# Optimization experiments

Measured on AMD Instinct MI355X. Metric: run time of the kernel, lower is better.

Reference implementation:

```python
import jax, jax.numpy as jnp
import numpy as np

N, E, MUL, ATTR, NBASIS = 30000, 480000, 32, 8, 8
AVG_NEIGH = 16.0
INV_SQRT3 = 1.0 / np.sqrt(3.0).astype(np.float32)  # wigner 3j (1,1,0)
LOG2 = float(np.log(2.0))


def ssp(x):
    # shifted softplus: softplus(x) - log(2)
    return jax.nn.softplus(x) - LOG2


def setup_inputs() -> dict:
    key = jax.random.key(0)
    ks = jax.random.split(key, 15)
    return {
        "node_s": jax.random.normal(ks[0], (N, MUL), jnp.float32),
        "node_v": jax.random.normal(ks[1], (N, MUL, 3), jnp.float32),
        "node_attr": jax.random.uniform(ks[2], (N, ATTR), jnp.float32),
        "edge_attr": jax.random.normal(ks[3], (E, 4), jnp.float32),       # [sh0 | sh1(3)]
        "edge_scalars": jax.random.uniform(ks[4], (E, NBASIS), jnp.float32),
        "W1_0": jax.random.normal(ks[5], (MUL, MUL), jnp.float32),
        "W1_1": jax.random.normal(ks[6], (MUL, MUL), jnp.float32),
        "Wfc1": jax.random.normal(ks[7], (NBASIS, NBASIS), jnp.float32),
        "Wfc2": jax.random.normal(ks[8], (NBASIS, 4 * MUL), jnp.float32),
        "W2_0": jax.random.normal(ks[9], (2 * MUL, MUL), jnp.float32),
        "W2_1": jax.random.normal(ks[10], (2 * MUL, MUL), jnp.float32),
        "Wsc0": jax.random.normal(ks[11], (MUL, ATTR, MUL), jnp.float32),
        "Wsc1": jax.random.normal(ks[12], (MUL, ATTR, MUL), jnp.float32),
        "edge_src": jax.random.randint(ks[13], (E,), 0, N, jnp.int32),
        "edge_dst": jax.random.randint(ks[14], (E,), 0, N, jnp.int32),
    }


def reference(node_s, node_v, node_attr, edge_attr, edge_scalars,
              W1_0, W1_1, Wfc1, Wfc2, W2_0, W2_1, Wsc0, Wsc1,
              edge_src, edge_dst):
    n_nodes, mul = node_s.shape
    # --- fc: radial MLP -> per-edge TP weights (shared_weights=False) ---
    h = ssp(edge_scalars @ Wfc1 * (1.0 / np.sqrt(Wfc1.shape[0])))
    w = h @ Wfc2 * (1.0 / np.sqrt(Wfc2.shape[0]))                 # [E, 4*MUL]
    w00, w01, w10, w11 = jnp.split(w, 4, axis=1)                  # instruction order
    # --- lin1: per-irrep linear (fan-in normalized) ---
    inv_m = 1.0 / np.sqrt(mul)
    x0 = node_s @ W1_0 * inv_m                                    # [N, MUL]
    x1 = jnp.einsum('nud,uw->nwd', node_v, W1_1) * inv_m          # [N, MUL, 3]
    # --- gather destination-node features per edge ---
    x0d, x1d = x0[edge_dst], x1[edge_dst]
    sh0, sh1 = edge_attr[:, :1], edge_attr[:, 1:4]
    # --- uvu tensor product with per-edge weights ---
    s_a = w00 * x0d * sh0                                         # 0e x 0e -> 0e
    s_b = w11 * jnp.einsum('eud,ed->eu', x1d, sh1) * INV_SQRT3    # 1o x 1o -> 0e
    v_a = (w01 * x0d)[:, :, None] * sh1[:, None, :]               # 0e x 1o -> 1o
    v_b = w10[:, :, None] * x1d * sh0[:, :, None]                 # 1o x 0e -> 1o
    mid_s = jnp.concatenate([s_a, s_b], axis=1)                   # [E, 64]  (64x0e)
    mid_v = jnp.concatenate([v_a, v_b], axis=1)                   # [E, 64, 3] (64x1o)
    # --- scatter-sum over edge_src, normalized by sqrt(avg_num_neighbors) ---
    inv_nb = 1.0 / np.sqrt(AVG_NEIGH)
    agg_s = jax.ops.segment_sum(mid_s, edge_src, num_segments=n_nodes) * inv_nb
    agg_v = jax.ops.segment_sum(mid_v, edge_src, num_segments=n_nodes) * inv_nb
    # --- lin2 ---
    inv_2m = 1.0 / np.sqrt(2.0 * mul)
    out0 = agg_s @ W2_0 * inv_2m                                  # [N, MUL]
    out1 = jnp.einsum('nud,uw->nwd', agg_v, W2_1) * inv_2m        # [N, MUL, 3]
    # --- self-connection: fully-connected TP (attr is scalar 8x0e) ---
    sc_norm = 1.0 / np.sqrt(mul * node_attr.shape[1])
    sc0 = jnp.einsum('nu,nv,uvw->nw', node_s, node_attr, Wsc0) * sc_norm
    sc1 = jnp.einsum('nud,nv,uvw->nwd', node_v, node_attr, Wsc1) * sc_norm
    o0 = out0 + sc0
    o1 = out1 + sc1
    return jnp.concatenate([o0, o1.reshape(n_nodes, mul * 3)], axis=1)  # [N, 128]
```

## Files before the change

kernel.cpp:

```cpp
#include <hip/hip_runtime.h>
#include <math.h>

#define N_NODES 30000
#define N_EDGES 480000

typedef __attribute__((ext_vector_type(8))) short short8;
typedef __attribute__((ext_vector_type(4))) float f32x4;
typedef __attribute__((ext_vector_type(2))) float f32x2;

__device__ __forceinline__ unsigned short f2bf(float f) {
    unsigned u = __float_as_uint(f);
    u += 0x7fff + ((u >> 16) & 1);
    return (unsigned short)(u >> 16);
}
__device__ __forceinline__ float bfLO(unsigned v) { return __uint_as_float(v << 16); }
__device__ __forceinline__ float bfHI(unsigned v) { return __uint_as_float(v & 0xffff0000u); }
__device__ __forceinline__ unsigned packbf(float a, float b) {
    return (unsigned)f2bf(a) | ((unsigned)f2bf(b) << 16);
}
__device__ __forceinline__ unsigned ptk(float a, float b) {
    return (__float_as_uint(a) >> 16) | (__float_as_uint(b) & 0xffff0000u);
}

union U8 { short8 v; unsigned u[4]; };
union C4 { f32x4 v; float f[4]; };

__global__ __launch_bounds__(256) void k_count(
    const int* __restrict__ edge_src,
    int* __restrict__ deg,
    int* __restrict__ epos)
{
    int e = blockIdx.x * 256 + threadIdx.x;
    epos[e] = atomicAdd(&deg[edge_src[e]], 1);
}

__global__ __launch_bounds__(256) void k_pre(
    const float* __restrict__ node_s,
    const float* __restrict__ node_v,
    const float* __restrict__ W1_0,
    const float* __restrict__ W1_1,
    const float* __restrict__ Wsc0,
    const float* __restrict__ Wsc1,
    const float* __restrict__ W2_0,
    const float* __restrict__ W2_1,
    const int* __restrict__ deg,
    int* __restrict__ offs,
    unsigned short* __restrict__ xnode,
    unsigned* __restrict__ bsc0,
    unsigned* __restrict__ bsc1,
    unsigned* __restrict__ b20,
    unsigned* __restrict__ b21)
{
    __shared__ __align__(16) char smem[15360];
    __shared__ int wsb[6];
    float* sVT = (float*)smem;
    float* sXo = (float*)(smem + 6400);
    int*   sdg = (int*)smem;
    int tid = threadIdx.x;

    if (blockIdx.x == 0) {
        int lane = tid & 63, wid = tid >> 6;
        int running = 0;
        for (int c = 0; c < N_NODES; c += 3840) {
            int size = min(3840, N_NODES - c);
#pragma unroll
            for (int k = 0; k < 15; ++k) {
                int i = tid + k * 256;
                sdg[i] = (i < size) ? deg[c + i] : 0;
            }
            __syncthreads();
            int bt = tid * 15;
            int s = 0;
#pragma unroll
            for (int k = 0; k < 15; ++k) s += sdg[bt + k];
            int inc = s;
#pragma unroll
            for (int d = 1; d < 64; d <<= 1) {
                int o = __shfl_up(inc, d, 64);
                if (lane >= d) inc += o;
            }
            if (lane == 63) wsb[wid] = inc;
            __syncthreads();
            if (tid == 0) {
                int t0 = 0;
#pragma unroll
                for (int w = 0; w < 4; ++w) { int v = wsb[w]; wsb[w] = t0; t0 += v; }
                wsb[4] = t0;
            }
            __syncthreads();
            int run2 = inc - s + wsb[wid] + running;
#pragma unroll
            for (int k = 0; k < 15; ++k) {
                int idx = bt + k;
                int gi = c + idx;
                int d = sdg[idx];
                if (gi < N_NODES) offs[gi] = run2;
                run2 += d;
            }
            running += wsb[4];
            __syncthreads();
        }
        if (tid == 0) offs[N_NODES] = N_EDGES;
        return;
    }

    if (blockIdx.x >= 1876) {
        int b = blockIdx.x - 1876;
        const float* Wm = (b == 0) ? Wsc0 : (b == 1) ? Wsc1 : (b == 2) ? W2_0 : W2_1;
        unsigned* dst = (b == 0) ? bsc0 : (b == 1) ? bsc1 : (b == 2) ? b20 : b21;
        float scale = (b < 2) ? 0.0625f : 0.03125f;
        int nu = (b < 2) ? 4096 : 1024;
        for (int idx = tid; idx < nu; idx += 256) {
            int jp = idx & 3;
            int lane = (idx >> 2) & 63;
            int ft = (idx >> 8) & 1;
            int kc = idx >> 9;
            int quad = lane >> 4, col = lane & 15;
            int k = kc * 32 + quad * 8 + jp * 2;
            int c = ft * 16 + col;
            dst[idx] = packbf(Wm[k * 32 + c] * scale, Wm[(k + 1) * 32 + c] * scale);
        }
        return;
    }

    int nbase = (blockIdx.x - 1) * 16;
    for (int i = tid; i < 1536; i += 256) {
        int nl = i / 96, r = i - nl * 96;
        int u = r / 3, d = r - u * 3;
        sVT[nl * 100 + d * 32 + u] = node_v[(size_t)nbase * 96 + i];
    }
    __syncthreads();

    int lane = tid & 63;
    int wv = tid >> 6;
    int col = lane & 15, quad = lane >> 4, m = lane & 15;

    const float* W1 = (wv == 0) ? W1_0 : W1_1;
    U8 bf0, bf1;
#pragma unroll
    for (int p = 0; p < 4; ++p) {
        int k = quad * 8 + 2 * p;
        bf0.u[p] = packbf(W1[k * 32 + col],      W1[(k + 1) * 32 + col]);
        bf1.u[p] = packbf(W1[k * 32 + col + 16], W1[(k + 1) * 32 + col + 16]);
    }

    U8 af;
    if (wv == 0) {
        const float* sp = node_s + (size_t)(nbase + m) * 32 + quad * 8;
        float4 a0 = *(const float4*)(sp);
        float4 a1 = *(const float4*)(sp + 4);
        af.u[0] = packbf(a0.x, a0.y); af.u[1] = packbf(a0.z, a0.w);
        af.u[2] = packbf(a1.x, a1.y); af.u[3] = packbf(a1.z, a1.w);
    } else {
        int R = 16 * (wv - 1) + m;
        int nl = R / 3, d = R - nl * 3;
        const float* vp = sVT + nl * 100 + d * 32 + quad * 8;
        af.u[0] = packbf(vp[0], vp[1]); af.u[1] = packbf(vp[2], vp[3]);
        af.u[2] = packbf(vp[4], vp[5]); af.u[3] = packbf(vp[6], vp[7]);
    }

    f32x4 acc0 = {0.f, 0.f, 0.f, 0.f};
    f32x4 acc1 = {0.f, 0.f, 0.f, 0.f};
    acc0 = __builtin_amdgcn_mfma_f32_16x16x32_bf16(af.v, bf0.v, acc0, 0, 0, 0);
    acc1 = __builtin_amdgcn_mfma_f32_16x16x32_bf16(af.v, bf1.v, acc1, 0, 0, 0);

    C4 c0, c1;
    c0.v = acc0; c1.v = acc1;
    if (wv == 0) {
#pragma unroll
        for (int r = 0; r < 4; ++r) {
            int nl = (quad << 2) + r;
            sXo[nl * 140 + col]      = c0.f[r];
            sXo[nl * 140 + col + 16] = c1.f[r];
        }
    } else {
#pragma unroll
        for (int r = 0; r < 4; ++r) {
            int R = 16 * (wv - 1) + (quad << 2) + r;
            int nl = R / 3, d = R - nl * 3;
            sXo[nl * 140 + (1 + d) * 34 + col]      = c0.f[r];
            sXo[nl * 140 + (1 + d) * 34 + col + 16] = c1.f[r];
        }
    }
    __syncthreads();

    const float inv_m = 0.1767766953f;
    for (int i = tid; i < 512; i += 256) {
        int nl = i >> 5, u = i & 31;
        const float* xp = sXo + nl * 140;
        uint2 pk;
        pk.x = packbf(xp[u] * inv_m,       xp[34 + u] * inv_m);
        pk.y = packbf(xp[68 + u] * inv_m,  xp[102 + u] * inv_m);
        *(uint2*)(xnode + (size_t)(nbase + nl) * 128 + u * 4) = pk;
    }
}

__global__ __launch_bounds__(256) void fill_kernel(
    const float* __restrict__ edge_attr,
    const float* __restrict__ edge_scalars,
    const float* __restrict__ Wfc1,
    const int* __restrict__ edge_src,
    const int* __restrict__ edge_dst,
    const int* __restrict__ offs,
    const int* __restrict__ epos,
    uint4* __restrict__ rec)
{
    __shared__ float sW[64];
    int tid = threadIdx.x;
    if (tid < 64) sW[tid] = Wfc1[tid];
    __syncthreads();

    int e = blockIdx.x * 256 + tid;
    float4 es0 = *(const float4*)(edge_scalars + (size_t)e * 8);
    float4 es1 = *(const float4*)(edge_scalars + (size_t)e * 8 + 4);
    float4 ea  = *(const float4*)(edge_attr + (size_t)e * 4);
    int src = edge_src[e];
    int dst = edge_dst[e];
    int pos = offs[src] + epos[e];

    const float inv8 = 0.3535533906f;
    float h[8];
#pragma unroll
    for (int i = 0; i < 8; ++i) {
        float acc = es0.x * sW[0 * 8 + i];
        acc = fmaf(es0.y, sW[1 * 8 + i], acc);
        acc = fmaf(es0.z, sW[2 * 8 + i], acc);
        acc = fmaf(es0.w, sW[3 * 8 + i], acc);
        acc = fmaf(es1.x, sW[4 * 8 + i], acc);
        acc = fmaf(es1.y, sW[5 * 8 + i], acc);
        acc = fmaf(es1.z, sW[6 * 8 + i], acc);
        acc = fmaf(es1.w, sW[7 * 8 + i], acc);
        acc *= inv8;
        float ax = fabsf(acc);
        float tt = __expf(-ax);
        h[i] = fmaxf(acc, 0.f) + __logf(1.f + tt) - 0.6931471806f;
    }
    uint4 r0, r1;
    r0.x = packbf(h[0], h[1]); r0.y = packbf(h[2], h[3]);
    r0.z = packbf(h[4], h[5]); r0.w = packbf(h[6], h[7]);
    r1.x = packbf(ea.x, ea.y); r1.y = packbf(ea.z, ea.w);
    r1.z = ((unsigned)dst) << 8;
    r1.w = 0;
    rec[2 * pos]     = r0;
    rec[2 * pos + 1] = r1;
}

struct GAcc {
    float sa, sb, va2, vb2;
    f32x2 va01, vb01;
};

__device__ __forceinline__ void gstep(
    uint4& RS0, uint4& RS1, uint2& XS, const uint4& RN1, uint2& XN,
    int& t, int cntH, int& pf, int L,
    const char* recc, const char* xbc,
    const f32x2* wfA, const f32x2* wfB, GAcc& g)
{
    float hv[8];
    hv[0] = bfLO(RS0.x); hv[1] = bfHI(RS0.x);
    hv[2] = bfLO(RS0.y); hv[3] = bfHI(RS0.y);
    hv[4] = bfLO(RS0.z); hv[5] = bfHI(RS0.z);
    hv[6] = bfLO(RS0.w); hv[7] = bfHI(RS0.w);
    float sh0  = bfLO(RS1.x), s1xe = bfHI(RS1.x);
    float s1ye = bfLO(RS1.y), s1ze = bfHI(RS1.y);
    float xv0 = bfLO(XS.x), xd0 = bfHI(XS.x);
    float xd1 = bfLO(XS.y), xd2 = bfHI(XS.y);
    bool ok = (t < cntH);

    RS0 = *(const uint4*)(recc + pf);
    RS1 = *(const uint4*)(recc + pf + 16);
    pf = min(pf + 64, L);
    XN = *(const uint2*)(xbc + RN1.z);

    f32x2 aA = {0.f, 0.f}, aB = {0.f, 0.f};
#pragma unroll
    for (int q = 0; q < 8; ++q) {
        f32x2 hh = {hv[q], hv[q]};
        aA = __builtin_elementwise_fma(hh, wfA[q], aA);
        aB = __builtin_elementwise_fma(hh, wfB[q], aB);
    }
    float a00 = ok ? aA.x : 0.f;
    float a01 = ok ? aA.y : 0.f;
    float a10 = ok ? aB.x : 0.f;
    float a11 = ok ? aB.y : 0.f;

    float dot = xd0 * s1xe + xd1 * s1ye + xd2 * s1ze;
    g.sa = fmaf(a00 * sh0, xv0, g.sa);
    g.sb = fmaf(a11, dot, g.sb);
    float w01x0 = a01 * xv0;
    float t10 = a10 * sh0;
    f32x2 wb = {w01x0, w01x0};
    f32x2 tb = {t10, t10};
    f32x2 s01 = {s1xe, s1ye};
    f32x2 xd01 = {xd0, xd1};
    g.va01 = __builtin_elementwise_fma(wb, s01, g.va01);
    g.vb01 = __builtin_elementwise_fma(tb, xd01, g.vb01);
    g.va2 = fmaf(w01x0, s1ze, g.va2);
    g.vb2 = fmaf(t10, xd2, g.vb2);
    ++t;
}

__global__ __launch_bounds__(256) void k_main(
    const int* __restrict__ offs,
    const uint4* __restrict__ rec,
    const float* __restrict__ Wfc2,
    const unsigned short* __restrict__ xnode,
    const float* __restrict__ node_s,
    const float* __restrict__ node_v,
    const float* __restrict__ node_attr,
    const unsigned* __restrict__ bsc0,
    const unsigned* __restrict__ bsc1,
    const unsigned* __restrict__ b20,
    const unsigned* __restrict__ b21,
    float* __restrict__ out)
{
    __shared__ float sS[16 * 33];
    __shared__ float sV[16 * 100];
    __shared__ unsigned short sAgg[16 * 264];
    int tid = threadIdx.x;

    int nbase = blockIdx.x * 16;
    for (int i = tid; i < 512; i += 256)
        sS[(i >> 5) * 33 + (i & 31)] = node_s[(size_t)nbase * 32 + i];
    for (int i = tid; i < 1536; i += 256)
        sV[(i / 96) * 100 + (i % 96)] = node_v[(size_t)nbase * 96 + i];

    int lane = tid & 63;
    int u = lane & 31;
    int half = lane >> 5;
    int wv = tid >> 6;

    const float inv8 = 0.3535533906f;
    const float i8s3 = 0.3535533906f * 0.5773502692f;
    f32x2 wfA[8], wfB[8];
#pragma unroll
    for (int q = 0; q < 8; ++q) {
        const float* wp = Wfc2 + q * 128 + u;
        wfA[q].x = wp[0]  * inv8;
        wfA[q].y = wp[32] * inv8;
        wfB[q].x = wp[64] * inv8;
        wfB[q].y = wp[96] * i8s3;
    }

    int nfirst = nbase + wv * 4;
    int beg = offs[nfirst];
#pragma unroll 1
    for (int j = 0; j < 4; ++j) {
        int end = offs[nfirst + j + 1];
        int cnt = end - beg;

        GAcc g;
        g.sa = 0.f; g.sb = 0.f; g.va2 = 0.f; g.vb2 = 0.f;
        g.va01 = (f32x2){0.f, 0.f};
        g.vb01 = (f32x2){0.f, 0.f};

        if (cnt > 0) {
            const char* recc = (const char*)rec;
            const char* xbc  = (const char*)xnode + u * 8;
            int T = (cnt + 1) >> 1;
            int cntH = (cnt + 1 - half) >> 1;
            int L = (end - 1) * 32;
            int b0 = (beg + half) * 32;

            uint4 r00, r01, r10, r11, r20, r21, r30, r31, r40, r41, r50, r51;
            uint2 x0, x1, x2, x3, x4, x5;
            x4.x = 0u; x4.y = 0u; x5.x = 0u; x5.y = 0u;
            int p;
            p = min(b0,       L); r00 = *(const uint4*)(recc + p); r01 = *(const uint4*)(recc + p + 16);
            p = min(b0 + 64,  L); r10 = *(const uint4*)(recc + p); r11 = *(const uint4*)(recc + p + 16);
            p = min(b0 + 128, L); r20 = *(const uint4*)(recc + p); r21 = *(const uint4*)(recc + p + 16);
            p = min(b0 + 192, L); r30 = *(const uint4*)(recc + p); r31 = *(const uint4*)(recc + p + 16);
            p = min(b0 + 256, L); r40 = *(const uint4*)(recc + p); r41 = *(const uint4*)(recc + p + 16);
            p = min(b0 + 320, L); r50 = *(const uint4*)(recc + p); r51 = *(const uint4*)(recc + p + 16);
            int pf = min(b0 + 384, L);
            x0 = *(const uint2*)(xbc + r01.z);
            x1 = *(const uint2*)(xbc + r11.z);
            x2 = *(const uint2*)(xbc + r21.z);
            x3 = *(const uint2*)(xbc + r31.z);

            int t = 0;
            int Tm = T - 5;
            while (t < Tm) {
                gstep(r00, r01, x0, r41, x4, t, cntH, pf, L, recc, xbc, wfA, wfB, g);
                gstep(r10, r11, x1, r51, x5, t, cntH, pf, L, recc, xbc, wfA, wfB, g);
                gstep(r20, r21, x2, r01, x0, t, cntH, pf, L, recc, xbc, wfA, wfB, g);
                gstep(r30, r31, x3, r11, x1, t, cntH, pf, L, recc, xbc, wfA, wfB, g);
                gstep(r40, r41, x4, r21, x2, t, cntH, pf, L, recc, xbc, wfA, wfB, g);
                gstep(r50, r51, x5, r31, x3, t, cntH, pf, L, recc, xbc, wfA, wfB, g);
            }
            if (t < T) gstep(r00, r01, x0, r41, x4, t, cntH, pf, L, recc, xbc, wfA, wfB, g);
            if (t < T) gstep(r10, r11, x1, r51, x5, t, cntH, pf, L, recc, xbc, wfA, wfB, g);
            if (t < T) gstep(r20, r21, x2, r01, x0, t, cntH, pf, L, recc, xbc, wfA, wfB, g);
            if (t < T) gstep(r30, r31, x3, r11, x1, t, cntH, pf, L, recc, xbc, wfA, wfB, g);
            if (t < T) gstep(r40, r41, x4, r21, x2, t, cntH, pf, L, recc, xbc, wfA, wfB, g);
        }

        g.sa      += __shfl_xor(g.sa, 32, 64);
        g.sb      += __shfl_xor(g.sb, 32, 64);
        g.va01.x  += __shfl_xor(g.va01.x, 32, 64);
        g.va01.y  += __shfl_xor(g.va01.y, 32, 64);
        g.vb01.x  += __shfl_xor(g.vb01.x, 32, 64);
        g.vb01.y  += __shfl_xor(g.vb01.y, 32, 64);
        g.va2     += __shfl_xor(g.va2, 32, 64);
        g.vb2     += __shfl_xor(g.vb2, 32, 64);

        int nl = wv * 4 + j;
        unsigned short* ap = sAgg + nl * 264;
        if (half == 0) {
            ap[u]       = f2bf(g.sa);
            ap[32 + u]  = f2bf(g.sb);
            ap[64 + u]  = f2bf(g.va01.x);
            ap[96 + u]  = f2bf(g.vb01.x);
        } else {
            ap[128 + u] = f2bf(g.va01.y);
            ap[160 + u] = f2bf(g.vb01.y);
            ap[192 + u] = f2bf(g.va2);
            ap[224 + u] = f2bf(g.vb2);
        }
        beg = end;
    }
    __syncthreads();

    int col = lane & 15;
    int quad = lane >> 4;
    int m = col;
    bool is_s = (wv == 0);
    int sub = wv - 1;

    const short* Bs = (const short*)(is_s ? bsc0 : bsc1);
    const short* B2 = (const short*)(is_s ? b20 : b21);

    int aBase, fbase, fstep, n_a;
    if (is_s) {
        aBase = m * 264;
        fbase = m * 33;
        fstep = 1;
        n_a = nbase + m;
    } else {
        int r16 = 16 * sub + m;
        int nl = r16 / 3;
        int dd = r16 - nl * 3;
        aBase = nl * 264 + 64 + 64 * dd;
        fbase = nl * 100 + dd;
        fstep = 3;
        n_a = nbase + nl;
    }
    float4 A0 = *(const float4*)(node_attr + (size_t)n_a * 8);
    float4 A1 = *(const float4*)(node_attr + (size_t)n_a * 8 + 4);
    float aa0 = A0.x, aa1 = A0.y, aa2 = A0.z, aa3 = A0.w;
    float aa4 = A1.x, aa5 = A1.y, aa6 = A1.z, aa7 = A1.w;

    f32x4 acc0 = {0.f, 0.f, 0.f, 0.f};
    f32x4 acc1 = {0.f, 0.f, 0.f, 0.f};

#pragma unroll
    for (int kc = 0; kc < 2; ++kc) {
        short8 af = *(const short8*)((const short*)sAgg + aBase + kc * 32 + quad * 8);
        short8 bf0 = *(const short8*)(B2 + ((kc * 2 + 0) * 64 + lane) * 8);
        short8 bf1 = *(const short8*)(B2 + ((kc * 2 + 1) * 64 + lane) * 8);
        acc0 = __builtin_amdgcn_mfma_f32_16x16x32_bf16(af, bf0, acc0, 0, 0, 0);
        acc1 = __builtin_amdgcn_mfma_f32_16x16x32_bf16(af, bf1, acc1, 0, 0, 0);
    }
    const float* Sf = is_s ? sS : sV;
#pragma unroll
    for (int kc = 0; kc < 8; ++kc) {
        int uu = kc * 4 + quad;
        float f = Sf[fbase + uu * fstep];
        U8 af;
        af.u[0] = ptk(f * aa0, f * aa1);
        af.u[1] = ptk(f * aa2, f * aa3);
        af.u[2] = ptk(f * aa4, f * aa5);
        af.u[3] = ptk(f * aa6, f * aa7);
        short8 bf0 = *(const short8*)(Bs + ((kc * 2 + 0) * 64 + lane) * 8);
        short8 bf1 = *(const short8*)(Bs + ((kc * 2 + 1) * 64 + lane) * 8);
        acc0 = __builtin_amdgcn_mfma_f32_16x16x32_bf16(af.v, bf0, acc0, 0, 0, 0);
        acc1 = __builtin_amdgcn_mfma_f32_16x16x32_bf16(af.v, bf1, acc1, 0, 0, 0);
    }

    C4 c0, c1;
    c0.v = acc0; c1.v = acc1;
    if (is_s) {
#pragma unroll
        for (int r = 0; r < 4; ++r) {
            int n = nbase + (quad << 2) + r;
            out[(size_t)n * 128 + col]      = c0.f[r];
            out[(size_t)n * 128 + col + 16] = c1.f[r];
        }
    } else {
#pragma unroll
        for (int r = 0; r < 4; ++r) {
            int rl = 16 * sub + (quad << 2) + r;
            int nn = rl / 3;
            int dd = rl - nn * 3;
            int n = nbase + nn;
            out[(size_t)n * 128 + 32 + 3 * col + dd]        = c0.f[r];
            out[(size_t)n * 128 + 32 + 3 * (col + 16) + dd] = c1.f[r];
        }
    }
}

extern "C" void kernel_launch(void* const* d_in, const int* in_sizes, int n_in,
                              void* d_out, int out_size, void* d_ws, size_t ws_size,
                              hipStream_t stream) {
    const float* node_s       = (const float*)d_in[0];
    const float* node_v       = (const float*)d_in[1];
    const float* node_attr    = (const float*)d_in[2];
    const float* edge_attr    = (const float*)d_in[3];
    const float* edge_scalars = (const float*)d_in[4];
    const float* W1_0 = (const float*)d_in[5];
    const float* W1_1 = (const float*)d_in[6];
    const float* Wfc1 = (const float*)d_in[7];
    const float* Wfc2 = (const float*)d_in[8];
    const float* W2_0 = (const float*)d_in[9];
    const float* W2_1 = (const float*)d_in[10];
    const float* Wsc0 = (const float*)d_in[11];
    const float* Wsc1 = (const float*)d_in[12];
    const int* edge_src = (const int*)d_in[13];
    const int* edge_dst = (const int*)d_in[14];

    char* ws = (char*)d_ws;
    unsigned short* xnode = (unsigned short*)(ws);
    uint4* rec            = (uint4*)(ws + 7680000);
    int* deg    = (int*)(ws + 23040000);
    int* offs   = (int*)(ws + 23160000);
    unsigned* bsc0 = (unsigned*)(ws + 23400064);
    unsigned* bsc1 = (unsigned*)(ws + 23416448);
    unsigned* b20  = (unsigned*)(ws + 23432832);
    unsigned* b21  = (unsigned*)(ws + 23436928);

    int* epos = (int*)d_out;

    hipMemsetAsync(deg, 0, (size_t)N_NODES * sizeof(int), stream);
    k_count<<<1875, 256, 0, stream>>>(edge_src, deg, epos);
    k_pre<<<1880, 256, 0, stream>>>(node_s, node_v, W1_0, W1_1, Wsc0, Wsc1,
                                    W2_0, W2_1, deg, offs, xnode,
                                    bsc0, bsc1, b20, b21);
    fill_kernel<<<1875, 256, 0, stream>>>(edge_attr, edge_scalars, Wfc1,
                                          edge_src, edge_dst, offs, epos, rec);
    k_main<<<1875, 256, 0, stream>>>(offs, rec, Wfc2, xnode,
                                     node_s, node_v, node_attr,
                                     bsc0, bsc1, b20, b21, (float*)d_out);
}
```

Measured before the change: 250.6 us.

## Fuse degree counting into preprocessing kernel with last-block prefix scan

Removes the separate atomic degree-count kernel and folds the per-edge atomicAdd into the node preprocessing blocks of k_pre. The exclusive scan over degrees now runs in whichever block finishes last, detected through a global done counter that is zeroed by the same widened memset. This saves one kernel launch and lets the scan overlap with the node linear work. In exchange, the scan becomes a serialized tail step that only starts after all blocks finish, and the code depends on acquire/release atomics being correct.

```diff
diff --git a/kernel.cpp b/kernel.cpp
--- a/kernel.cpp
+++ b/kernel.cpp
@@ -24,15 +24,6 @@
 
 union U8 { short8 v; unsigned u[4]; };
 union C4 { f32x4 v; float f[4]; };
-
-__global__ __launch_bounds__(256) void k_count(
-    const int* __restrict__ edge_src,
-    int* __restrict__ deg,
-    int* __restrict__ epos)
-{
-    int e = blockIdx.x * 256 + threadIdx.x;
-    epos[e] = atomicAdd(&deg[edge_src[e]], 1);
-}
 
 __global__ __launch_bounds__(256) void k_pre(
     const float* __restrict__ node_s,
@@ -43,8 +34,11 @@
     const float* __restrict__ Wsc1,
     const float* __restrict__ W2_0,
     const float* __restrict__ W2_1,
-    const int* __restrict__ deg,
+    const int* __restrict__ edge_src,
+    int* __restrict__ deg,
     int* __restrict__ offs,
+    int* __restrict__ done,
+    int* __restrict__ epos,
     unsigned short* __restrict__ xnode,
     unsigned* __restrict__ bsc0,
     unsigned* __restrict__ bsc1,
@@ -53,20 +47,124 @@
 {
     __shared__ __align__(16) char smem[15360];
     __shared__ int wsb[6];
+    __shared__ int sOld;
     float* sVT = (float*)smem;
     float* sXo = (float*)(smem + 6400);
     int*   sdg = (int*)smem;
     int tid = threadIdx.x;
-
-    if (blockIdx.x == 0) {
-        int lane = tid & 63, wid = tid >> 6;
+    int lane = tid & 63;
+
+    if (blockIdx.x >= 1875) {
+        int b = blockIdx.x - 1875;
+        const float* Wm = (b == 0) ? Wsc0 : (b == 1) ? Wsc1 : (b == 2) ? W2_0 : W2_1;
+        unsigned* dst = (b == 0) ? bsc0 : (b == 1) ? bsc1 : (b == 2) ? b20 : b21;
+        float scale = (b < 2) ? 0.0625f : 0.03125f;
+        int nu = (b < 2) ? 4096 : 1024;
+        for (int idx = tid; idx < nu; idx += 256) {
+            int jp = idx & 3;
+            int ln = (idx >> 2) & 63;
+            int ft = (idx >> 8) & 1;
+            int kc = idx >> 9;
+            int quad = ln >> 4, col = ln & 15;
+            int k = kc * 32 + quad * 8 + jp * 2;
+            int c = ft * 16 + col;
+            dst[idx] = packbf(Wm[k * 32 + c] * scale, Wm[(k + 1) * 32 + c] * scale);
+        }
+    } else {
+        int e = blockIdx.x * 256 + tid;
+        epos[e] = atomicAdd(&deg[edge_src[e]], 1);
+
+        int nbase = blockIdx.x * 16;
+        for (int i = tid; i < 1536; i += 256) {
+            int nl = i / 96, r = i - nl * 96;
+            int u = r / 3, d = r - u * 3;
+            sVT[nl * 100 + d * 32 + u] = node_v[(size_t)nbase * 96 + i];
+        }
+        __syncthreads();
+
+        int wv = tid >> 6;
+        int col = lane & 15, quad = lane >> 4, m = lane & 15;
+
+        const float* W1 = (wv == 0) ? W1_0 : W1_1;
+        U8 bf0, bf1;
+#pragma unroll
+        for (int p = 0; p < 4; ++p) {
+            int k = quad * 8 + 2 * p;
+            bf0.u[p] = packbf(W1[k * 32 + col],      W1[(k + 1) * 32 + col]);
+            bf1.u[p] = packbf(W1[k * 32 + col + 16], W1[(k + 1) * 32 + col + 16]);
+        }
+
+        U8 af;
+        if (wv == 0) {
+            const float* sp = node_s + (size_t)(nbase + m) * 32 + quad * 8;
+            float4 a0 = *(const float4*)(sp);
+            float4 a1 = *(const float4*)(sp + 4);
+            af.u[0] = packbf(a0.x, a0.y); af.u[1] = packbf(a0.z, a0.w);
+            af.u[2] = packbf(a1.x, a1.y); af.u[3] = packbf(a1.z, a1.w);
+        } else {
+            int R = 16 * (wv - 1) + m;
+            int nl = R / 3, d = R - nl * 3;
+            const float* vp = sVT + nl * 100 + d * 32 + quad * 8;
+            af.u[0] = packbf(vp[0], vp[1]); af.u[1] = packbf(vp[2], vp[3]);
+            af.u[2] = packbf(vp[4], vp[5]); af.u[3] = packbf(vp[6], vp[7]);
+        }
+
+        f32x4 acc0 = {0.f, 0.f, 0.f, 0.f};
+        f32x4 acc1 = {0.f, 0.f, 0.f, 0.f};
+        acc0 = __builtin_amdgcn_mfma_f32_16x16x32_bf16(af.v, bf0.v, acc0, 0, 0, 0);
+        acc1 = __builtin_amdgcn_mfma_f32_16x16x32_bf16(af.v, bf1.v, acc1, 0, 0, 0);
+
+        C4 c0, c1;
+        c0.v = acc0; c1.v = acc1;
+        if (wv == 0) {
+#pragma unroll
+            for (int r = 0; r < 4; ++r) {
+                int nl = (quad << 2) + r;
+                sXo[nl * 140 + col]      = c0.f[r];
+                sXo[nl * 140 + col + 16] = c1.f[r];
+            }
+        } else {
+#pragma unroll
+            for (int r = 0; r < 4; ++r) {
+                int R = 16 * (wv - 1) + (quad << 2) + r;
+                int nl = R / 3, d = R - nl * 3;
+                sXo[nl * 140 + (1 + d) * 34 + col]      = c0.f[r];
+                sXo[nl * 140 + (1 + d) * 34 + col + 16] = c1.f[r];
+            }
+        }
+        __syncthreads();
+
+        const float inv_m = 0.1767766953f;
+        for (int i = tid; i < 512; i += 256) {
+            int nl = i >> 5, u = i & 31;
+            const float* xp = sXo + nl * 140;
+            uint2 pk;
+            pk.x = packbf(xp[u] * inv_m,       xp[34 + u] * inv_m);
+            pk.y = packbf(xp[68 + u] * inv_m,  xp[102 + u] * inv_m);
+            *(uint2*)(xnode + (size_t)(nbase + nl) * 128 + u * 4) = pk;
+        }
+    }
+
+    __syncthreads();
+    if (tid == 0)
+        sOld = __hip_atomic_fetch_add(done, 1, __ATOMIC_ACQ_REL,
+                                      __HIP_MEMORY_SCOPE_AGENT);
+    __syncthreads();
+    if (sOld != 1878) return;
+
+    {
+        int wid = tid >> 6;
         int running = 0;
         for (int c = 0; c < N_NODES; c += 3840) {
             int size = min(3840, N_NODES - c);
+            __syncthreads();
 #pragma unroll
             for (int k = 0; k < 15; ++k) {
                 int i = tid + k * 256;
-                sdg[i] = (i < size) ? deg[c + i] : 0;
+                sdg[i] = (i < size)
+                    ? __hip_atomic_load(&deg[c + i], __ATOMIC_RELAXED,
+                                        __HIP_MEMORY_SCOPE_AGENT)
+                    : 0;
             }
             __syncthreads();
             int bt = tid * 15;
@@ -98,100 +196,8 @@
                 run2 += d;
             }
             running += wsb[4];
-            __syncthreads();
         }
         if (tid == 0) offs[N_NODES] = N_EDGES;
-        return;
-    }
-
-    if (blockIdx.x >= 1876) {
-        int b = blockIdx.x - 1876;
-        const float* Wm = (b == 0) ? Wsc0 : (b == 1) ? Wsc1 : (b == 2) ? W2_0 : W2_1;
-        unsigned* dst = (b == 0) ? bsc0 : (b == 1) ? bsc1 : (b == 2) ? b20 : b21;
-        float scale = (b < 2) ? 0.0625f : 0.03125f;
-        int nu = (b < 2) ? 4096 : 1024;
-        for (int idx = tid; idx < nu; idx += 256) {
-            int jp = idx & 3;
-            int lane = (idx >> 2) & 63;
-            int ft = (idx >> 8) & 1;
-            int kc = idx >> 9;
-            int quad = lane >> 4, col = lane & 15;
-            int k = kc * 32 + quad * 8 + jp * 2;
-            int c = ft * 16 + col;
-            dst[idx] = packbf(Wm[k * 32 + c] * scale, Wm[(k + 1) * 32 + c] * scale);
-        }
-        return;
-    }
-
-    int nbase = (blockIdx.x - 1) * 16;
-    for (int i = tid; i < 1536; i += 256) {
-        int nl = i / 96, r = i - nl * 96;
-        int u = r / 3, d = r - u * 3;
-        sVT[nl * 100 + d * 32 + u] = node_v[(size_t)nbase * 96 + i];
-    }
-    __syncthreads();
-
-    int lane = tid & 63;
-    int wv = tid >> 6;
-    int col = lane & 15, quad = lane >> 4, m = lane & 15;
-
-    const float* W1 = (wv == 0) ? W1_0 : W1_1;
-    U8 bf0, bf1;
-#pragma unroll
-    for (int p = 0; p < 4; ++p) {
-        int k = quad * 8 + 2 * p;
-        bf0.u[p] = packbf(W1[k * 32 + col],      W1[(k + 1) * 32 + col]);
-        bf1.u[p] = packbf(W1[k * 32 + col + 16], W1[(k + 1) * 32 + col + 16]);
-    }
-
-    U8 af;
-    if (wv == 0) {
-        const float* sp = node_s + (size_t)(nbase + m) * 32 + quad * 8;
-        float4 a0 = *(const float4*)(sp);
-        float4 a1 = *(const float4*)(sp + 4);
-        af.u[0] = packbf(a0.x, a0.y); af.u[1] = packbf(a0.z, a0.w);
-        af.u[2] = packbf(a1.x, a1.y); af.u[3] = packbf(a1.z, a1.w);
-    } else {
-        int R = 16 * (wv - 1) + m;
-        int nl = R / 3, d = R - nl * 3;
-        const float* vp = sVT + nl * 100 + d * 32 + quad * 8;
-        af.u[0] = packbf(vp[0], vp[1]); af.u[1] = packbf(vp[2], vp[3]);
-        af.u[2] = packbf(vp[4], vp[5]); af.u[3] = packbf(vp[6], vp[7]);
-    }
-
-    f32x4 acc0 = {0.f, 0.f, 0.f, 0.f};
-    f32x4 acc1 = {0.f, 0.f, 0.f, 0.f};
-    acc0 = __builtin_amdgcn_mfma_f32_16x16x32_bf16(af.v, bf0.v, acc0, 0, 0, 0);
-    acc1 = __builtin_amdgcn_mfma_f32_16x16x32_bf16(af.v, bf1.v, acc1, 0, 0, 0);
-
-    C4 c0, c1;
-    c0.v = acc0; c1.v = acc1;
-    if (wv == 0) {
-#pragma unroll
-        for (int r = 0; r < 4; ++r) {
-            int nl = (quad << 2) + r;
-            sXo[nl * 140 + col]      = c0.f[r];
-            sXo[nl * 140 + col + 16] = c1.f[r];
-        }
-    } else {
-#pragma unroll
-        for (int r = 0; r < 4; ++r) {
-            int R = 16 * (wv - 1) + (quad << 2) + r;
-            int nl = R / 3, d = R - nl * 3;
-            sXo[nl * 140 + (1 + d) * 34 + col]      = c0.f[r];
-            sXo[nl * 140 + (1 + d) * 34 + col + 16] = c1.f[r];
-        }
-    }
-    __syncthreads();
-
-    const float inv_m = 0.1767766953f;
-    for (int i = tid; i < 512; i += 256) {
-        int nl = i >> 5, u = i & 31;
-        const float* xp = sXo + nl * 140;
-        uint2 pk;
-        pk.x = packbf(xp[u] * inv_m,       xp[34 + u] * inv_m);
-        pk.y = packbf(xp[68 + u] * inv_m,  xp[102 + u] * inv_m);
-        *(uint2*)(xnode + (size_t)(nbase + nl) * 128 + u * 4) = pk;
     }
 }
 
@@ -523,6 +529,7 @@
     uint4* rec            = (uint4*)(ws + 7680000);
     int* deg    = (int*)(ws + 23040000);
     int* offs   = (int*)(ws + 23160000);
+    int* done   = (int*)(ws + 23280004);
     unsigned* bsc0 = (unsigned*)(ws + 23400064);
     unsigned* bsc1 = (unsigned*)(ws + 23416448);
     unsigned* b20  = (unsigned*)(ws + 23432832);
@@ -530,11 +537,10 @@
 
     int* epos = (int*)d_out;
 
-    hipMemsetAsync(deg, 0, (size_t)N_NODES * sizeof(int), stream);
-    k_count<<<1875, 256, 0, stream>>>(edge_src, deg, epos);
-    k_pre<<<1880, 256, 0, stream>>>(node_s, node_v, W1_0, W1_1, Wsc0, Wsc1,
-                                    W2_0, W2_1, deg, offs, xnode,
-                                    bsc0, bsc1, b20, b21);
+    hipMemsetAsync(deg, 0, 240008, stream);
+    k_pre<<<1879, 256, 0, stream>>>(node_s, node_v, W1_0, W1_1, Wsc0, Wsc1,
+                                    W2_0, W2_1, edge_src, deg, offs, done,
+                                    epos, xnode, bsc0, bsc1, b20, b21);
     fill_kernel<<<1875, 256, 0, stream>>>(edge_attr, edge_scalars, Wfc1,
                                           edge_src, edge_dst, offs, epos, rec);
     k_main<<<1875, 256, 0, stream>>>(offs, rec, Wfc2, xnode,
```

Result: slower. 308.2 us (+23.0%).
